# Performance work log

Hardware: AMD Instinct MI355X
Metric: run time of the kernel (lower is better)

Reference implementation:

```python
import jax, jax.numpy as jnp
import numpy as np

N_NODES = 50000
DIM = 64
HEADS = 4
N_EDGES = 800000
NEG_SLOPE = 0.2  # PyG GATConv default


def setup_inputs() -> dict:
    key = jax.random.key(0)
    ks = jax.random.split(key, 8)
    H, C = HEADS, DIM
    embedding = jax.random.normal(ks[0], (N_NODES, DIM), dtype=jnp.float32)
    graph = jax.random.randint(ks[1], (2, N_EDGES), 0, N_NODES, dtype=jnp.int64)
    s = 1.0 / np.sqrt(DIM)
    # GATConv params: shared source/target linear (PyG uses one lin when in_channels is int)
    W = jax.random.normal(ks[2], (DIM, H * C), dtype=jnp.float32) * s
    att_src = jax.random.normal(ks[3], (H, C), dtype=jnp.float32) * s
    att_dst = jax.random.normal(ks[4], (H, C), dtype=jnp.float32) * s
    bias = jnp.zeros((H * C,), dtype=jnp.float32)
    # dense: Linear(dim*heads -> dim)
    dense_w = jax.random.normal(ks[5], (H * C, DIM), dtype=jnp.float32) / np.sqrt(H * C)
    dense_b = jnp.zeros((DIM,), dtype=jnp.float32)
    return {"embedding": embedding, "graph": graph, "W": W, "att_src": att_src,
            "att_dst": att_dst, "bias": bias, "dense_w": dense_w, "dense_b": dense_b}


def reference(embedding, graph, W, att_src, att_dst, bias, dense_w, dense_b):
    N, D = embedding.shape
    H, C = att_src.shape
    # linear projection, per-head view: [N, H, C]
    x = (embedding @ W).reshape(N, H, C)
    # add self loops (PyG default add_self_loops=True)
    ar = jnp.arange(N, dtype=graph.dtype)
    src = jnp.concatenate([graph[0], ar])  # [E+N]
    dst = jnp.concatenate([graph[1], ar])
    # per-node attention logits, gathered per edge
    a_src = jnp.einsum('nhc,hc->nh', x, att_src)  # [N, H]
    a_dst = jnp.einsum('nhc,hc->nh', x, att_dst)
    alpha = jax.nn.leaky_relu(a_src[src] + a_dst[dst], NEG_SLOPE)  # [E, H]
    # segment softmax over destination nodes
    amax = jax.ops.segment_max(alpha, dst, num_segments=N)  # [N, H]
    amax = jnp.where(jnp.isfinite(amax), amax, 0.0)
    ex = jnp.exp(alpha - amax[dst])
    denom = jax.ops.segment_sum(ex, dst, num_segments=N)
    coef = ex / (denom[dst] + 1e-16)  # [E, H]
    # weighted scatter-aggregate of source features
    msg = x[src] * coef[:, :, None]  # [E, H, C]
    agg = jax.ops.segment_sum(msg, dst, num_segments=N)  # [N, H, C]
    gat_out = agg.reshape(N, H * C) + bias  # concat heads + bias
    return gat_out @ dense_w + dense_b  # [N, D]
```

## Files before the change

### kernel.cpp

```cpp
#include <hip/hip_runtime.h>
#include <hip/hip_fp16.h>
#include <cfloat>
#include <cmath>

#define DIM 64
#define HEADS 4
#define NEG 0.2f
#define CAP 64
#define NPART 8
#define BPP 96

typedef int v4i __attribute__((ext_vector_type(4)));

__device__ __forceinline__ float lrelu(float a) { return a > 0.0f ? a : NEG * a; }

__device__ __forceinline__ unsigned pack_half2(float a, float b) {
    return (unsigned)__half_as_ushort(__float2half(a)) |
           ((unsigned)__half_as_ushort(__float2half(b)) << 16);
}

__global__ __launch_bounds__(256) void prep_kernel(
        const float* __restrict__ W, const float* __restrict__ dw,
        const float* __restrict__ att_s, const float* __restrict__ att_d,
        const float* __restrict__ bias, const float* __restrict__ db,
        const float* __restrict__ emb,
        __half* __restrict__ M2h, float* __restrict__ bvec,
        float* __restrict__ a_src, float* __restrict__ a_dst,
        unsigned* __restrict__ embh, int* __restrict__ cnt, int N) {
    const int b = blockIdx.x, t = threadIdx.x;
    if (b < 64) {
        __shared__ float s_W[256];
        s_W[t] = W[b * 256 + t];
        __syncthreads();
        const int h = t >> 6, j = t & 63;
        float s = 0.f;
        for (int c = 0; c < 64; c++)
            s = fmaf(s_W[h * 64 + c], dw[(h * 64 + c) * 64 + j], s);
        M2h[(size_t)(h * 64 + b) * 64 + j] = __float2half(s);
    } else if (b == 64) {
        __shared__ float s_p[256];
        const int j = t & 63, kq = t >> 6;
        float p = 0.f;
        for (int k = kq * 64; k < kq * 64 + 64; k++)
            p = fmaf(bias[k], dw[k * 64 + j], p);
        s_p[t] = p;
        __syncthreads();
        if (t < 64)
            bvec[t] = s_p[t] + s_p[64 + t] + s_p[128 + t] + s_p[192 + t] + db[t];
    } else {
        __shared__ float s_e[64 * 68];
        __shared__ float s_vs[256], s_vd[256];
        const int n0 = (b - 65) * 64;
        {
            const int d = t >> 2, h = t & 3;
            const float4* w4 = (const float4*)(W + d * 256 + h * 64);
            const float4* s4 = (const float4*)(att_s + h * 64);
            const float4* d4 = (const float4*)(att_d + h * 64);
            float vs = 0.f, vd = 0.f;
#pragma unroll
            for (int k = 0; k < 16; k++) {
                float4 w = w4[k], as = s4[k], ad = d4[k];
                vs = fmaf(w.x, as.x, fmaf(w.y, as.y, fmaf(w.z, as.z, fmaf(w.w, as.w, vs))));
                vd = fmaf(w.x, ad.x, fmaf(w.y, ad.y, fmaf(w.z, ad.z, fmaf(w.w, ad.w, vd))));
            }
            s_vs[h * 64 + d] = vs;
            s_vd[h * 64 + d] = vd;
        }
#pragma unroll
        for (int r = 0; r < 4; r++) {
            int idx = (r * 256 + t) * 4;
            int i = idx >> 6, d = idx & 63;
            int row = min(n0 + i, N - 1);
            *(float4*)(s_e + i * 68 + d) = *(const float4*)(emb + (size_t)row * 64 + d);
        }
        __syncthreads();
        const int node = t >> 2, h = t & 3;
        const float* er = s_e + node * 68;
        float as = 0.f, ad = 0.f;
#pragma unroll
        for (int g = 0; g < 16; g++) {
            float4 ev = *(const float4*)(er + 4 * g);
            float4 vs = *(const float4*)(s_vs + h * 64 + 4 * g);
            float4 vd = *(const float4*)(s_vd + h * 64 + 4 * g);
            as = fmaf(ev.x, vs.x, fmaf(ev.y, vs.y, fmaf(ev.z, vs.z, fmaf(ev.w, vs.w, as))));
            ad = fmaf(ev.x, vd.x, fmaf(ev.y, vd.y, fmaf(ev.z, vd.z, fmaf(ev.w, vd.w, ad))));
        }
        const int n = n0 + node;
        if (n < N) {
            a_src[(size_t)n * 4 + h] = as;
            a_dst[(size_t)n * 4 + h] = ad;
            const float* ep = s_e + node * 68 + h * 16;
            uint4 u0, u1;
            u0.x = pack_half2(ep[0],  ep[1]);  u0.y = pack_half2(ep[2],  ep[3]);
            u0.z = pack_half2(ep[4],  ep[5]);  u0.w = pack_half2(ep[6],  ep[7]);
            u1.x = pack_half2(ep[8],  ep[9]);  u1.y = pack_half2(ep[10], ep[11]);
            u1.z = pack_half2(ep[12], ep[13]); u1.w = pack_half2(ep[14], ep[15]);
            unsigned* dst = embh + (size_t)n * 32 + h * 8;
            *(uint4*)dst = u0;
            *(uint4*)(dst + 4) = u1;
        }
        if (t < 64 && n0 + t < N) cnt[n0 + t] = 0;
    }
}

__global__ __launch_bounds__(256) void fill_kernel(
        const int* __restrict__ gsrc, const int* __restrict__ gdst,
        int* __restrict__ cnt, int* __restrict__ adj, int E, int N) {
    const int t = threadIdx.x;
    const int part = blockIdx.x & (NPART - 1);
    const int slot = blockIdx.x >> 3;
    const int lo = (int)((long long)part * N / NPART);
    const int hi = (int)((long long)(part + 1) * N / NPART);
    const unsigned span = (unsigned)(hi - lo);
    const int quads = (E + 3) >> 2;
    const int stride = BPP * 256;

    for (int q = slot * 256 + t; q < quads; q += stride) {
        const int e0 = q * 4;
        v4i s4, d4;
        if (e0 + 3 < E) {
            d4 = __builtin_nontemporal_load((const v4i*)(gdst + e0));
            s4 = __builtin_nontemporal_load((const v4i*)(gsrc + e0));
        } else {
#pragma unroll
            for (int k = 0; k < 4; k++) {
                const int e = e0 + k;
                d4[k] = (e < E) ? gdst[e] : -1;
                s4[k] = (e < E) ? gsrc[e] : 0;
            }
        }
#pragma unroll
        for (int k = 0; k < 4; k++) {
            const int d = d4[k];
            if ((unsigned)(d - lo) < span) {
                const int pos = atomicAdd(&cnt[d], 1);
                if (pos < CAP) adj[(size_t)d * CAP + pos] = s4[k];
            }
        }
    }
}

__global__ __launch_bounds__(256) void aggregate_kernel(
        const int* __restrict__ cnt, const int* __restrict__ adj,
        const float* __restrict__ a_src, const float* __restrict__ a_dst,
        const unsigned* __restrict__ embh, unsigned* __restrict__ zbuf, int N) {
    const int t = threadIdx.x;
    const int l = t & 63;
    const int dd = blockIdx.x * 4 + (t >> 6);
    if (dd >= N) return;
    const int d = __builtin_amdgcn_readfirstlane(dd);
    const int hl = l >> 4;
    const int lh = l & 48;
    const int q = l & 15;
    const int deg = min(__builtin_amdgcn_readfirstlane(cnt[d]), CAP);
    const unsigned* el = embh + 2 * q;

    int my_src = 0;
    if (l < deg) my_src = adj[(size_t)d * CAP + l];

    const float ad = a_dst[(size_t)d * 4 + hl];

    float pv0, pv1, pv2, pv3;
    {
#define PRE_PV(G, PV) {                                                    \
            const int e_ = (G) * 16 + q;                                   \
            const int se_ = __shfl(my_src, e_, 64);                        \
            float pe_ = 0.f;                                               \
            if (e_ < deg)                                                  \
                pe_ = __expf(lrelu(a_src[(size_t)se_ * 4 + hl] + ad));     \
            (PV) = pe_; }
        PRE_PV(0, pv0); PRE_PV(1, pv1); PRE_PV(2, pv2); PRE_PV(3, pv3);
#undef PRE_PV
    }

    float den, zx, zy, zz, zw;
    {
        const float p = __expf(lrelu(a_src[(size_t)d * 4 + hl] + ad));
        const uint2 v = *(const uint2*)(el + (size_t)d * 32);
        const float2 f0 = __half22float2(*(const __half2*)&v.x);
        const float2 f1 = __half22float2(*(const __half2*)&v.y);
        den = p;
        zx = p * f0.x; zy = p * f0.y; zz = p * f1.x; zw = p * f1.y;
    }

#define AGG_EDGE(PG, I, J) {                                               \
        const int si_ = __builtin_amdgcn_readlane(my_src, (I));            \
        const float pe_ = __shfl((PG), lh + (J), 64);                      \
        const uint2 vv_ = *(const uint2*)(el + (size_t)si_ * 32);          \
        const float2 g0_ = __half22float2(*(const __half2*)&vv_.x);        \
        const float2 g1_ = __half22float2(*(const __half2*)&vv_.y);        \
        den += pe_;                                                        \
        zx = fmaf(pe_, g0_.x, zx); zy = fmaf(pe_, g0_.y, zy);              \
        zz = fmaf(pe_, g1_.x, zz); zw = fmaf(pe_, g1_.y, zw); }

#define AGG_GROUP(G, PG) {                                                 \
        const int base_ = (G) * 16;                                        \
        if (base_ < deg) {                                                 \
            const int mp_ = min(16, ((deg - base_) + 3) & ~3);             \
            _Pragma("unroll 1")                                            \
            for (int j = 0; j < mp_; j += 4) {                             \
                AGG_EDGE(PG, base_ + j + 0, j + 0);                        \
                AGG_EDGE(PG, base_ + j + 1, j + 1);                        \
                AGG_EDGE(PG, base_ + j + 2, j + 2);                        \
                AGG_EDGE(PG, base_ + j + 3, j + 3);                        \
            }                                                              \
        } }

    AGG_GROUP(0, pv0);
    AGG_GROUP(1, pv1);
    AGG_GROUP(2, pv2);
    AGG_GROUP(3, pv3);
#undef AGG_GROUP
#undef AGG_EDGE

    const float inv = 1.0f / (den + 1e-16f);
    uint2 u;
    u.x = pack_half2(zx * inv, zy * inv);
    u.y = pack_half2(zz * inv, zw * inv);
    *(uint2*)(zbuf + (size_t)dd * 128 + 2 * l) = u;
}

__global__ __launch_bounds__(256) void outgemm_kernel(
        const unsigned* __restrict__ zbuf, const unsigned* __restrict__ M2u,
        const float* __restrict__ bvec, float* __restrict__ out, int N) {
    __shared__ unsigned s_m[8192];
    __shared__ unsigned s_z[8192];
    const int t = threadIdx.x;
    const int n0 = blockIdx.x * 64;

#pragma unroll
    for (int r = 0; r < 8; r++)
        *(uint4*)(s_m + (r * 256 + t) * 4) = *(const uint4*)(M2u + (r * 256 + t) * 4);
#pragma unroll
    for (int r = 0; r < 8; r++) {
        const int idx = r * 256 + t;
        const int row = idx >> 5, c4 = (idx & 31) * 4;
        const int n = n0 + row;
        uint4 v = make_uint4(0u, 0u, 0u, 0u);
        if (n < N) v = *(const uint4*)(zbuf + (size_t)n * 128 + c4);
        *(uint4*)(s_z + row * 128 + c4) = v;
    }
    __syncthreads();

    const int l = t & 63;
    const int wq = t >> 6;
    const int g = l >> 4, q = l & 15;
    const unsigned* zrow = s_z + (wq * 16) * 128 + g * 32;

    float4 acc[16];
#pragma unroll
    for (int i = 0; i < 16; i++) acc[i] = make_float4(0.f, 0.f, 0.f, 0.f);

#pragma unroll 2
    for (int i = 0; i < 32; i++) {
        const int kk = (i + 8 * g) & 31;
        const int k = g * 64 + 2 * kk;
        const uint2 ma = *(const uint2*)(s_m + k * 32 + 2 * q);
        const uint2 mb = *(const uint2*)(s_m + (k + 1) * 32 + 2 * q);
        const float2 a0 = __half22float2(*(const __half2*)&ma.x);
        const float2 a1 = __half22float2(*(const __half2*)&ma.y);
        const float2 b0 = __half22float2(*(const __half2*)&mb.x);
        const float2 b1 = __half22float2(*(const __half2*)&mb.y);
#pragma unroll
        for (int n = 0; n < 16; n++) {
            const unsigned zp = zrow[n * 128 + kk];
            const float2 zf = __half22float2(*(const __half2*)&zp);
            acc[n].x = fmaf(zf.x, a0.x, acc[n].x);
            acc[n].y = fmaf(zf.x, a0.y, acc[n].y);
            acc[n].z = fmaf(zf.x, a1.x, acc[n].z);
            acc[n].w = fmaf(zf.x, a1.y, acc[n].w);
            acc[n].x = fmaf(zf.y, b0.x, acc[n].x);
            acc[n].y = fmaf(zf.y, b0.y, acc[n].y);
            acc[n].z = fmaf(zf.y, b1.x, acc[n].z);
            acc[n].w = fmaf(zf.y, b1.y, acc[n].w);
        }
    }

    const float4 bv = *(const float4*)(bvec + 4 * q);
#pragma unroll
    for (int n = 0; n < 16; n++) {
        float4 r = acc[n];
        r.x += __shfl_xor(r.x, 16, 64); r.y += __shfl_xor(r.y, 16, 64);
        r.z += __shfl_xor(r.z, 16, 64); r.w += __shfl_xor(r.w, 16, 64);
        r.x += __shfl_xor(r.x, 32, 64); r.y += __shfl_xor(r.y, 32, 64);
        r.z += __shfl_xor(r.z, 32, 64); r.w += __shfl_xor(r.w, 32, 64);
        const int nn = n0 + wq * 16 + n;
        if (l < 16 && nn < N) {
            float4 o;
            o.x = r.x + bv.x; o.y = r.y + bv.y; o.z = r.z + bv.z; o.w = r.w + bv.w;
            *(float4*)(out + (size_t)nn * 64 + 4 * q) = o;
        }
    }
}

extern "C" void kernel_launch(void* const* d_in, const int* in_sizes, int n_in,
                              void* d_out, int out_size, void* d_ws, size_t ws_size,
                              hipStream_t stream) {
    const float* emb   = (const float*)d_in[0];
    const int*   graph = (const int*)d_in[1];
    const float* W     = (const float*)d_in[2];
    const float* att_s = (const float*)d_in[3];
    const float* att_d = (const float*)d_in[4];
    const float* bias  = (const float*)d_in[5];
    const float* dw    = (const float*)d_in[6];
    const float* db    = (const float*)d_in[7];
    float* out = (float*)d_out;

    const int N = in_sizes[0] / DIM;
    const int E = in_sizes[1] / 2;
    const int* gsrc = graph;
    const int* gdst = graph + E;

    unsigned* zbuf = (unsigned*)d_ws;
    int* adj       = (int*)(zbuf + (size_t)N * 128);
    unsigned* embh = (unsigned*)(adj + (size_t)N * CAP);
    float* a_src   = (float*)(embh + (size_t)N * 32);
    float* a_dst   = a_src + (size_t)N * 4;
    __half* M2h    = (__half*)(a_dst + (size_t)N * 4);
    float* bvec    = (float*)((unsigned*)M2h + 8192);
    int*   cnt     = (int*)(bvec + 64);

    const int PB = (N + 63) / 64;
    const int FILLB = NPART * BPP;

    hipLaunchKernelGGL(prep_kernel, dim3(65 + PB), dim3(256), 0, stream,
                       W, dw, att_s, att_d, bias, db, emb,
                       M2h, bvec, a_src, a_dst, embh, cnt, N);
    hipLaunchKernelGGL(fill_kernel, dim3(FILLB), dim3(256), 0, stream,
                       gsrc, gdst, cnt, adj, E, N);
    hipLaunchKernelGGL(aggregate_kernel, dim3((N + 3) / 4), dim3(256), 0, stream,
                       cnt, adj, a_src, a_dst, embh, zbuf, N);
    hipLaunchKernelGGL(outgemm_kernel, dim3(PB), dim3(256), 0, stream,
                       zbuf, (const unsigned*)M2h, bvec, out, N);
}
```

Measured before the change: 217.8 us.

## Fuse neighbor aggregation with output GEMM via shared-memory staging

```diff
diff --git a/kernel.cpp b/kernel.cpp
--- a/kernel.cpp
+++ b/kernel.cpp
@@ -140,28 +140,38 @@
     }
 }
 
-__global__ __launch_bounds__(256) void aggregate_kernel(
+__global__ __launch_bounds__(256) void agg_out_kernel(
         const int* __restrict__ cnt, const int* __restrict__ adj,
         const float* __restrict__ a_src, const float* __restrict__ a_dst,
-        const unsigned* __restrict__ embh, unsigned* __restrict__ zbuf, int N) {
+        const unsigned* __restrict__ embh, const unsigned* __restrict__ M2u,
+        const float* __restrict__ bvec, float* __restrict__ out, int N) {
+    __shared__ unsigned s_z[8192];
     const int t = threadIdx.x;
     const int l = t & 63;
-    const int dd = blockIdx.x * 4 + (t >> 6);
-    if (dd >= N) return;
-    const int d = __builtin_amdgcn_readfirstlane(dd);
+    const int wq = __builtin_amdgcn_readfirstlane(t >> 6);
+    const int n0 = blockIdx.x * 64;
     const int hl = l >> 4;
     const int lh = l & 48;
     const int q = l & 15;
-    const int deg = min(__builtin_amdgcn_readfirstlane(cnt[d]), CAP);
     const unsigned* el = embh + 2 * q;
 
-    int my_src = 0;
-    if (l < deg) my_src = adj[(size_t)d * CAP + l];
-
-    const float ad = a_dst[(size_t)d * 4 + hl];
-
-    float pv0, pv1, pv2, pv3;
-    {
+    for (int it = 0; it < 16; ++it) {
+        const int dd = n0 + wq * 16 + it;
+        unsigned* zslot = s_z + (wq * 16 + it) * 128 + 2 * l;
+        if (dd >= N) {
+            *(uint2*)zslot = make_uint2(0u, 0u);
+            continue;
+        }
+        const int d = __builtin_amdgcn_readfirstlane(dd);
+        const int deg = min(__builtin_amdgcn_readfirstlane(cnt[d]), CAP);
+
+        int my_src = 0;
+        if (l < deg) my_src = adj[(size_t)d * CAP + l];
+
+        const float ad = a_dst[(size_t)d * 4 + hl];
+
+        float pv0, pv1, pv2, pv3;
+        {
 #define PRE_PV(G, PV) {                                                    \
             const int e_ = (G) * 16 + q;                                   \
             const int se_ = __shfl(my_src, e_, 64);                        \
@@ -169,19 +179,19 @@
             if (e_ < deg)                                                  \
                 pe_ = __expf(lrelu(a_src[(size_t)se_ * 4 + hl] + ad));     \
             (PV) = pe_; }
-        PRE_PV(0, pv0); PRE_PV(1, pv1); PRE_PV(2, pv2); PRE_PV(3, pv3);
+            PRE_PV(0, pv0); PRE_PV(1, pv1); PRE_PV(2, pv2); PRE_PV(3, pv3);
 #undef PRE_PV
-    }
-
-    float den, zx, zy, zz, zw;
-    {
-        const float p = __expf(lrelu(a_src[(size_t)d * 4 + hl] + ad));
-        const uint2 v = *(const uint2*)(el + (size_t)d * 32);
-        const float2 f0 = __half22float2(*(const __half2*)&v.x);
-        const float2 f1 = __half22float2(*(const __half2*)&v.y);
-        den = p;
-        zx = p * f0.x; zy = p * f0.y; zz = p * f1.x; zw = p * f1.y;
-    }
+        }
+
+        float den, zx, zy, zz, zw;
+        {
+            const float p = __expf(lrelu(a_src[(size_t)d * 4 + hl] + ad));
+            const uint2 v = *(const uint2*)(el + (size_t)d * 32);
+            const float2 f0 = __half22float2(*(const __half2*)&v.x);
+            const float2 f1 = __half22float2(*(const __half2*)&v.y);
+            den = p;
+            zx = p * f0.x; zy = p * f0.y; zz = p * f1.x; zw = p * f1.y;
+        }
 
 #define AGG_EDGE(PG, I, J) {                                               \
         const int si_ = __builtin_amdgcn_readlane(my_src, (I));            \
@@ -206,45 +216,22 @@
             }                                                              \
         } }
 
-    AGG_GROUP(0, pv0);
-    AGG_GROUP(1, pv1);
-    AGG_GROUP(2, pv2);
-    AGG_GROUP(3, pv3);
+        AGG_GROUP(0, pv0);
+        AGG_GROUP(1, pv1);
+        AGG_GROUP(2, pv2);
+        AGG_GROUP(3, pv3);
 #undef AGG_GROUP
 #undef AGG_EDGE
 
-    const float inv = 1.0f / (den + 1e-16f);
-    uint2 u;
-    u.x = pack_half2(zx * inv, zy * inv);
-    u.y = pack_half2(zz * inv, zw * inv);
-    *(uint2*)(zbuf + (size_t)dd * 128 + 2 * l) = u;
-}
-
-__global__ __launch_bounds__(256) void outgemm_kernel(
-        const unsigned* __restrict__ zbuf, const unsigned* __restrict__ M2u,
-        const float* __restrict__ bvec, float* __restrict__ out, int N) {
-    __shared__ unsigned s_m[8192];
-    __shared__ unsigned s_z[8192];
-    const int t = threadIdx.x;
-    const int n0 = blockIdx.x * 64;
-
-#pragma unroll
-    for (int r = 0; r < 8; r++)
-        *(uint4*)(s_m + (r * 256 + t) * 4) = *(const uint4*)(M2u + (r * 256 + t) * 4);
-#pragma unroll
-    for (int r = 0; r < 8; r++) {
-        const int idx = r * 256 + t;
-        const int row = idx >> 5, c4 = (idx & 31) * 4;
-        const int n = n0 + row;
-        uint4 v = make_uint4(0u, 0u, 0u, 0u);
-        if (n < N) v = *(const uint4*)(zbuf + (size_t)n * 128 + c4);
-        *(uint4*)(s_z + row * 128 + c4) = v;
+        const float inv = 1.0f / (den + 1e-16f);
+        uint2 u;
+        u.x = pack_half2(zx * inv, zy * inv);
+        u.y = pack_half2(zz * inv, zw * inv);
+        *(uint2*)zslot = u;
     }
     __syncthreads();
 
-    const int l = t & 63;
-    const int wq = t >> 6;
-    const int g = l >> 4, q = l & 15;
+    const int g = l >> 4;
     const unsigned* zrow = s_z + (wq * 16) * 128 + g * 32;
 
     float4 acc[16];
@@ -255,8 +242,8 @@
     for (int i = 0; i < 32; i++) {
         const int kk = (i + 8 * g) & 31;
         const int k = g * 64 + 2 * kk;
-        const uint2 ma = *(const uint2*)(s_m + k * 32 + 2 * q);
-        const uint2 mb = *(const uint2*)(s_m + (k + 1) * 32 + 2 * q);
+        const uint2 ma = *(const uint2*)(M2u + k * 32 + 2 * q);
+        const uint2 mb = *(const uint2*)(M2u + (k + 1) * 32 + 2 * q);
         const float2 a0 = __half22float2(*(const __half2*)&ma.x);
         const float2 a1 = __half22float2(*(const __half2*)&ma.y);
         const float2 b0 = __half22float2(*(const __half2*)&mb.x);
@@ -311,8 +298,7 @@
     const int* gsrc = graph;
     const int* gdst = graph + E;
 
-    unsigned* zbuf = (unsigned*)d_ws;
-    int* adj       = (int*)(zbuf + (size_t)N * 128);
+    int* adj       = (int*)d_ws;
     unsigned* embh = (unsigned*)(adj + (size_t)N * CAP);
     float* a_src   = (float*)(embh + (size_t)N * 32);
     float* a_dst   = a_src + (size_t)N * 4;
@@ -328,8 +314,7 @@
                        M2h, bvec, a_src, a_dst, embh, cnt, N);
     hipLaunchKernelGGL(fill_kernel, dim3(FILLB), dim3(256), 0, stream,
                        gsrc, gdst, cnt, adj, E, N);
-    hipLaunchKernelGGL(aggregate_kernel, dim3((N + 3) / 4), dim3(256), 0, stream,
-                       cnt, adj, a_src, a_dst, embh, zbuf, N);
-    hipLaunchKernelGGL(outgemm_kernel, dim3(PB), dim3(256), 0, stream,
-                       zbuf, (const unsigned*)M2h, bvec, out, N);
-}
+    hipLaunchKernelGGL(agg_out_kernel, dim3(PB), dim3(256), 0, stream,
+                       cnt, adj, a_src, a_dst, embh, (const unsigned*)M2h,
+                       bvec, out, N);
+}
```

New measurement: 271.0 us. 1.24x slower.
